# Performance work log

Measured on AMD Instinct MI355X. Metric: run time of the kernel, lower is better.

Reference implementation:

```python
import jax, jax.numpy as jnp
import numpy as np

KH, KW = 5, 5  # kernel; stride=1, padding=0, dilation=1 per init_kwargs


def _unfold(x, kh, kw):
    # torch.nn.functional.unfold with stride=1, pad=0, dil=1, channel-major
    # ordering: out channel index = c*kh*kw + i*kw + j
    B, C, H, W = x.shape
    oh, ow = H - kh + 1, W - kw + 1
    patches = jnp.stack(
        [x[:, :, i:i + oh, j:j + ow] for i in range(kh) for j in range(kw)],
        axis=2,
    )  # [B, C, kh*kw, oh, ow]
    return patches.reshape(B, C * kh * kw, oh, ow)


def _sample_spikes(inp_conv, T):
    # multinomial(replacement=True) over the Cf channel dim per (b, x, y)
    logits = jnp.log(inp_conv.transpose(0, 2, 3, 1))  # [B, OH, OW, Cf]
    B, OH, OW, _ = logits.shape
    return jax.random.categorical(
        jax.random.key(42), logits[:, None], axis=-1, shape=(B, T, OH, OW)
    )  # [B, T, OH, OW] int


def setup_inputs() -> dict:
    key = jax.random.key(0)
    ks = jax.random.split(key, 6)
    B, C, H, W = 32, 24, 28, 28
    OH, OW = 24, 24
    Hn = 128  # number of hidden neurons
    T = 96    # number of spikes
    Cf = C * KH * KW  # 600
    return {
        "input": jax.random.uniform(ks[0], (B, C, H, W), jnp.float32, 0.01, 1.0),
        "epsilon_xy": jax.random.uniform(ks[1], (OH, OW, KH, KW), jnp.float32, 0.1, 1.0),
        "epsilon_0": jax.random.uniform(ks[2], (1,), jnp.float32, 0.5, 1.0),
        "epsilon_t": jax.random.uniform(ks[3], (T,), jnp.float32, 0.5, 1.0),
        "weights": jax.random.uniform(ks[4], (Cf, Hn), jnp.float32, 0.0, 1.0),
        "h_initial": jax.random.uniform(ks[5], (Hn,), jnp.float32, 0.5, 1.0),
        "number_of_spikes": T,
    }


def reference(input, epsilon_xy, epsilon_0, epsilon_t, weights, h_initial,
              number_of_spikes):
    T = int(number_of_spikes)
    B, C = input.shape[0], input.shape[1]
    inp_conv = _unfold(input, KH, KW)              # [B, Cf, OH, OW]
    spikes = _sample_spikes(inp_conv, T)           # [B, T, OH, OW]
    OH, OW = spikes.shape[2], spikes.shape[3]

    # epsilon_xy_convolved: value independent of input channel c,
    # index c*KH*KW + k -> epsilon_xy[x, y] flat at k. Stored as [OH, OW, Cf].
    eps_conv = jnp.tile(epsilon_xy.reshape(OH, OW, KH * KW), (1, 1, C))
    eps0 = epsilon_0[0]

    # Normalized recurrence: g = h / epsilon_scale (exactly equivalent to the
    # original h/epsilon_scale bookkeeping, including the overflow-rescale branch):
    #   g' = (g + eps_sub * (W[s]*g) / sum(W[s]*g)) / (1 + eps_sub)
    Hn = h_initial.shape[0]
    g0 = jnp.broadcast_to(h_initial, (B, OH, OW, Hn)).astype(jnp.float32)

    def step(g, xs):
        s, et = xs                                  # s: [B, OH, OW]
        wg = weights[s] * g                         # [B, OH, OW, Hn]
        denom = jnp.sum(wg, axis=-1, keepdims=True)  # [B, OH, OW, 1]
        eps = jnp.take_along_axis(eps_conv[None], s[..., None], axis=-1)
        eps_sub = eps * (et * eps0)                 # [B, OH, OW, 1]
        factor = jnp.nan_to_num(eps_sub / denom, nan=0.0, posinf=0.0, neginf=0.0)
        g = (g + wg * factor) / (1.0 + eps_sub)
        return g, None

    g, _ = jax.lax.scan(step, g0, (jnp.moveaxis(spikes, 1, 0), epsilon_t[:T]))
    return jnp.moveaxis(g, 3, 1)                    # [B, Hn, OH, OW]
```

## Files before the change

### kernel.cpp

```cpp
#include <hip/hip_runtime.h>
#include <stdint.h>

constexpr int Bn = 32, Cc = 24, Hh = 28, Ww = 28;
constexpr int OHt = 24, OWt = 24;
constexpr int CF = 600, HN = 128, TT = 96;
constexpr int NPIX = OHt * OWt;
constexpr int NSAMP = Bn * TT * NPIX;
constexpr int NLOG = Bn * Cc * Hh * Ww;

__device__ __forceinline__ uint32_t threefry_0_42_pre(uint32_t x1) {
  const uint32_t ks1 = 42u, ks2 = 0x1BD11BF0u;
  uint32_t x0 = x1;
  x1 = __builtin_rotateleft32(x1, 13) ^ x0;
  x0 += x1; x1 = __builtin_rotateleft32(x1, 15) ^ x0;
  x0 += x1; x1 = __builtin_rotateleft32(x1, 26) ^ x0;
  x0 += x1; x1 = __builtin_rotateleft32(x1,  6) ^ x0;
  x0 += ks1; x1 += ks2 + 1u;
  x0 += x1; x1 = __builtin_rotateleft32(x1, 17) ^ x0;
  x0 += x1; x1 = __builtin_rotateleft32(x1, 29) ^ x0;
  x0 += x1; x1 = __builtin_rotateleft32(x1, 16) ^ x0;
  x0 += x1; x1 = __builtin_rotateleft32(x1, 24) ^ x0;
  x0 += ks2; x1 += 2u;
  x0 += x1; x1 = __builtin_rotateleft32(x1, 13) ^ x0;
  x0 += x1; x1 = __builtin_rotateleft32(x1, 15) ^ x0;
  x0 += x1; x1 = __builtin_rotateleft32(x1, 26) ^ x0;
  x0 += x1; x1 = __builtin_rotateleft32(x1,  6) ^ x0;
  x1 += ks1 + 3u;
  x0 += x1; x1 = __builtin_rotateleft32(x1, 17) ^ x0;
  x0 += x1; x1 = __builtin_rotateleft32(x1, 29) ^ x0;
  x0 += x1; x1 = __builtin_rotateleft32(x1, 16) ^ x0;
  x0 += x1; x1 = __builtin_rotateleft32(x1, 24) ^ x0;
  x0 += ks1; x1 += ks2 + 4u;
  x0 += x1; x1 = __builtin_rotateleft32(x1, 13) ^ x0;
  x0 += x1; x1 = __builtin_rotateleft32(x1, 15) ^ x0;
  x0 += x1; x1 = __builtin_rotateleft32(x1, 26) ^ x0;
  x0 += x1; x1 = __builtin_rotateleft32(x1,  6) ^ x0;
  x0 += ks2; x1 += 5u;
  return x0 ^ x1;
}

__global__ __launch_bounds__(256) void k_log(const float* __restrict__ in,
                                             float* __restrict__ lp) {
  int i = blockIdx.x * 256 + threadIdx.x;
  if (i < NLOG) lp[i] = logf(in[i]);
}

__global__ __launch_bounds__(256) void k_lpmax(const float* __restrict__ lp,
                                               float* __restrict__ out) {
  int pid = blockIdx.x * 256 + threadIdx.x;
  if (pid >= Bn * NPIX) return;
  int y = pid % OWt;
  int x = (pid / OWt) % OHt;
  int b = pid / NPIX;
  const float* p = lp + (b * Cc) * (Hh * Ww) + x * Ww + y;
  float m = -3.0e38f;
  for (int c = 0; c < Cc; ++c) {
    const float* pc = p + c * (Hh * Ww);
    #pragma unroll
    for (int ki = 0; ki < 5; ++ki)
      #pragma unroll
      for (int kj = 0; kj < 5; ++kj) m = fmaxf(m, pc[ki * Ww + kj]);
  }
  out[pid] = m;
}

__device__ __forceinline__ uint32_t mkthr(float bgap) {
  float g3 = bgap - 0.00390625f;
  float e1 = __expf(-g3) * 1.0000153f;
  float ul = __expf(-e1) * 0.9999847f;
  int kt = (int)(ul * 8388608.0f) - 64;
  return (kt < 1) ? 0u : ((uint32_t)kt << 9);
}

constexpr int NBIN = 640;

__device__ __forceinline__ void upd(uint32_t bits, float lp, float lpmax,
                                    int cf, float& best, int& bi,
                                    uint32_t& thr, const uint32_t* tab) {
  if (bits < thr) return;
  uint32_t key = bits >> 9;
  float f = __uint_as_float(key | 0x3f800000u) - 1.0f;
  float u = (f == 0.0f) ? 1.17549435e-38f : f;
  float l1 = logf(u);
  float v = -logf(-l1) + lp;
  if (v > best) {
    best = v;
    bi = cf;
    float bg = v - lpmax;
    int bin = (int)__builtin_fmaf(bg, 32.0f, 255.0f);
    if (bin < 0) thr = 0u;
    else thr = tab[bin > (NBIN - 1) ? (NBIN - 1) : bin];
  }
}

__global__ __launch_bounds__(256) void k_sample(const float* __restrict__ logp,
                                                const float* __restrict__ lpmaxa,
                                                int* __restrict__ spikes) {
  __shared__ uint32_t thr_tab[NBIN];
  for (int i = threadIdx.x; i < NBIN; i += 256)
    thr_tab[i] = mkthr(__builtin_fmaf((float)i, 0.03125f, -8.0f));
  __syncthreads();

  int tid = blockIdx.x * 256 + threadIdx.x;
  int y = tid % OWt;
  int x = (tid / OWt) % OHt;
  int t = (tid / NPIX) % 48;
  int b = tid / (NPIX * 48);
  int sid1 = ((b * TT + t) * OHt + x) * OWt + y;
  int sid2 = sid1 + 48 * NPIX;
  uint32_t base1 = (uint32_t)sid1 * 600u + 42u;
  uint32_t base2 = (uint32_t)sid2 * 600u + 42u;
  const float* lpb = logp + (b * Cc) * (Hh * Ww) + x * Ww + y;
  float lpmax = lpmaxa[(b * OHt + x) * OWt + y];
  float best1 = -1e30f, best2 = -1e30f;
  int bi1 = 0, bi2 = 0;
  uint32_t thr1 = 0u, thr2 = 0u;
  int cf = 0;
  #pragma unroll 1
  for (int c = 0; c < Cc; ++c) {
    const float* lpc = lpb + c * (Hh * Ww);
    #pragma unroll
    for (int ki = 0; ki < 5; ++ki) {
      #pragma unroll
      for (int kj = 0; kj < 5; ++kj) {
        float lp = lpc[ki * Ww + kj];
        uint32_t bits1 = threefry_0_42_pre(base1 + (uint32_t)cf);
        uint32_t bits2 = threefry_0_42_pre(base2 + (uint32_t)cf);
        upd(bits1, lp, lpmax, cf, best1, bi1, thr1, thr_tab);
        upd(bits2, lp, lpmax, cf, best2, bi2, thr2, thr_tab);
        ++cf;
      }
    }
  }
  spikes[sid1] = bi1;
  spikes[sid2] = bi2;
}

__global__ __launch_bounds__(256) void k_recur(
    const int* __restrict__ spikes, const float* __restrict__ weights,
    const float* __restrict__ eps_xy, const float* __restrict__ eps_t,
    const float* __restrict__ eps0p, const float* __restrict__ h_init,
    float* __restrict__ out) {
  int wid = blockIdx.x * 4 + (threadIdx.x >> 6);
  int lane = threadIdx.x & 63;
  int y = wid % OWt;
  int x = (wid / OWt) % OHt;
  int b = wid / NPIX;
  float g0 = h_init[lane];
  float g1 = h_init[lane + 64];
  float e0 = eps0p[0];
  const int* sp = spikes + (b * TT) * NPIX + x * OWt + y;
  const float* ex = eps_xy + (x * OWt + y) * 25;
  for (int t = 0; t < TT; ++t) {
    int s = sp[t * NPIX];
    const float* wr = weights + s * HN;
    float wg0 = wr[lane] * g0;
    float wg1 = wr[lane + 64] * g1;
    float sum = wg0 + wg1;
    #pragma unroll
    for (int off = 32; off > 0; off >>= 1) sum += __shfl_xor(sum, off, 64);
    float es = ex[s % 25] * (eps_t[t] * e0);
    float factor = es / sum;
    if (!__builtin_isfinite(factor)) factor = 0.0f;
    float d = 1.0f + es;
    g0 = (g0 + wg0 * factor) / d;
    g1 = (g1 + wg1 * factor) / d;
  }
  out[((b * HN + lane) * OHt + x) * OWt + y] = g0;
  out[((b * HN + lane + 64) * OHt + x) * OWt + y] = g1;
}

extern "C" void kernel_launch(void* const* d_in, const int* in_sizes, int n_in,
                              void* d_out, int out_size, void* d_ws, size_t ws_size,
                              hipStream_t stream) {
  const float* input   = (const float*)d_in[0];
  const float* eps_xy  = (const float*)d_in[1];
  const float* eps0    = (const float*)d_in[2];
  const float* eps_t   = (const float*)d_in[3];
  const float* weights = (const float*)d_in[4];
  const float* h_init  = (const float*)d_in[5];

  float* logp = (float*)d_ws;
  int* spikes = (int*)((char*)d_ws + NLOG * sizeof(float));
  float* lpmax = (float*)d_out;

  k_log<<<(NLOG + 255) / 256, 256, 0, stream>>>(input, logp);
  k_lpmax<<<(Bn * NPIX + 255) / 256, 256, 0, stream>>>(logp, lpmax);
  k_sample<<<(NSAMP / 2) / 256, 256, 0, stream>>>(logp, lpmax, spikes);
  k_recur<<<(Bn * NPIX) / 4, 256, 0, stream>>>(spikes, weights, eps_xy, eps_t,
                                               eps0, h_init, (float*)d_out);
}
```

Before: 2.381 ms.

## Replace exact running argmax with approximate candidate filtering and exact resolve pass

The Gumbel-max sampling loop now keeps a running bound built from fast log2 approximations instead of exact logf values. It uses that bound to pick a threshold per element and records the indices of candidates that pass in a shared-memory list. A second pass recomputes exact values for only those candidates, falling back to a full rescan if the list overflows. This removes the separate lpmax kernel and most exact-log work on the hot path, at the cost of shared-memory stores, per-element table lookups, a partly rolled inner loop, and a redundant threefry recomputation in the resolve pass.

```diff
diff --git a/kernel.cpp b/kernel.cpp
--- a/kernel.cpp
+++ b/kernel.cpp
@@ -7,6 +7,8 @@
 constexpr int NPIX = OHt * OWt;
 constexpr int NSAMP = Bn * TT * NPIX;
 constexpr int NLOG = Bn * Cc * Hh * Ww;
+constexpr int NBIN = 640;
+constexpr int KREC = 24;
 
 __device__ __forceinline__ uint32_t threefry_0_42_pre(uint32_t x1) {
   const uint32_t ks1 = 42u, ks2 = 0x1BD11BF0u;
@@ -45,25 +47,6 @@
   if (i < NLOG) lp[i] = logf(in[i]);
 }
 
-__global__ __launch_bounds__(256) void k_lpmax(const float* __restrict__ lp,
-                                               float* __restrict__ out) {
-  int pid = blockIdx.x * 256 + threadIdx.x;
-  if (pid >= Bn * NPIX) return;
-  int y = pid % OWt;
-  int x = (pid / OWt) % OHt;
-  int b = pid / NPIX;
-  const float* p = lp + (b * Cc) * (Hh * Ww) + x * Ww + y;
-  float m = -3.0e38f;
-  for (int c = 0; c < Cc; ++c) {
-    const float* pc = p + c * (Hh * Ww);
-    #pragma unroll
-    for (int ki = 0; ki < 5; ++ki)
-      #pragma unroll
-      for (int kj = 0; kj < 5; ++kj) m = fmaxf(m, pc[ki * Ww + kj]);
-  }
-  out[pid] = m;
-}
-
 __device__ __forceinline__ uint32_t mkthr(float bgap) {
   float g3 = bgap - 0.00390625f;
   float e1 = __expf(-g3) * 1.0000153f;
@@ -72,31 +55,71 @@
   return (kt < 1) ? 0u : ((uint32_t)kt << 9);
 }
 
-constexpr int NBIN = 640;
-
-__device__ __forceinline__ void upd(uint32_t bits, float lp, float lpmax,
-                                    int cf, float& best, int& bi,
-                                    uint32_t& thr, const uint32_t* tab) {
-  if (bits < thr) return;
+__device__ __forceinline__ float exact_v(uint32_t bits, float lp) {
   uint32_t key = bits >> 9;
   float f = __uint_as_float(key | 0x3f800000u) - 1.0f;
   float u = (f == 0.0f) ? 1.17549435e-38f : f;
   float l1 = logf(u);
-  float v = -logf(-l1) + lp;
-  if (v > best) {
-    best = v;
-    bi = cf;
-    float bg = v - lpmax;
-    int bin = (int)__builtin_fmaf(bg, 32.0f, 255.0f);
-    if (bin < 0) thr = 0u;
-    else thr = tab[bin > (NBIN - 1) ? (NBIN - 1) : bin];
-  }
+  return -logf(-l1) + lp;
+}
+
+__device__ __forceinline__ void rec_upd(uint32_t bits, float lp, float& bA32,
+                                        int& cnt, uint16_t (*recs)[256],
+                                        const uint32_t* __restrict__ tab,
+                                        int cf) {
+  float t = __builtin_fmaf(lp, -32.0f, bA32);
+  t = fminf(fmaxf(t, 0.0f), 639.0f);
+  uint32_t thr = tab[(int)t];
+  if (bits >= thr) {
+    uint32_t key = bits >> 9;
+    float f = __uint_as_float(key | 0x3f800000u) - 1.0f;
+    float u = (f == 0.0f) ? 1.17549435e-38f : f;
+    float lg = __log2f(u);
+    float n = __log2f(-lg);
+    float vh = __builtin_fmaf(-0.6931471805599453f, n, lp);
+    bA32 = fmaxf(bA32, __builtin_fmaf(vh, 32.0f, 266.7284135f));
+    int slot = cnt < KREC - 1 ? cnt : KREC - 1;
+    recs[slot][threadIdx.x] = (uint16_t)cf;
+    ++cnt;
+  }
+}
+
+__device__ __forceinline__ int resolve(int cnt, const uint16_t (*recs)[256],
+                                       uint32_t base,
+                                       const float* __restrict__ lpb) {
+  float best = -1e30f;
+  int bi = 0;
+  if (cnt <= KREC) {
+    for (int j = 0; j < cnt; ++j) {
+      int cf = recs[j][threadIdx.x];
+      int c = cf / 25;
+      int r = cf - c * 25;
+      int ki = r / 5;
+      int kj = r - ki * 5;
+      float lp = lpb[c * (Hh * Ww) + ki * Ww + kj];
+      float v = exact_v(threefry_0_42_pre(base + (uint32_t)cf), lp);
+      if (v > best) { best = v; bi = cf; }
+    }
+  } else {
+    int cf = 0;
+    for (int c = 0; c < Cc; ++c) {
+      const float* lpc = lpb + c * (Hh * Ww);
+      for (int ki = 0; ki < 5; ++ki)
+        for (int kj = 0; kj < 5; ++kj) {
+          float v = exact_v(threefry_0_42_pre(base + (uint32_t)cf),
+                            lpc[ki * Ww + kj]);
+          if (v > best) { best = v; bi = cf; }
+          ++cf;
+        }
+    }
+  }
+  return bi;
 }
 
 __global__ __launch_bounds__(256) void k_sample(const float* __restrict__ logp,
-                                                const float* __restrict__ lpmaxa,
                                                 int* __restrict__ spikes) {
   __shared__ uint32_t thr_tab[NBIN];
+  __shared__ uint16_t rec[2][KREC][256];
   for (int i = threadIdx.x; i < NBIN; i += 256)
     thr_tab[i] = mkthr(__builtin_fmaf((float)i, 0.03125f, -8.0f));
   __syncthreads();
@@ -111,29 +134,27 @@
   uint32_t base1 = (uint32_t)sid1 * 600u + 42u;
   uint32_t base2 = (uint32_t)sid2 * 600u + 42u;
   const float* lpb = logp + (b * Cc) * (Hh * Ww) + x * Ww + y;
-  float lpmax = lpmaxa[(b * OHt + x) * OWt + y];
-  float best1 = -1e30f, best2 = -1e30f;
-  int bi1 = 0, bi2 = 0;
-  uint32_t thr1 = 0u, thr2 = 0u;
+  float bA1 = -3.0e38f, bA2 = -3.0e38f;
+  int cnt1 = 0, cnt2 = 0;
   int cf = 0;
   #pragma unroll 1
   for (int c = 0; c < Cc; ++c) {
     const float* lpc = lpb + c * (Hh * Ww);
-    #pragma unroll
+    #pragma unroll 1
     for (int ki = 0; ki < 5; ++ki) {
       #pragma unroll
       for (int kj = 0; kj < 5; ++kj) {
         float lp = lpc[ki * Ww + kj];
         uint32_t bits1 = threefry_0_42_pre(base1 + (uint32_t)cf);
         uint32_t bits2 = threefry_0_42_pre(base2 + (uint32_t)cf);
-        upd(bits1, lp, lpmax, cf, best1, bi1, thr1, thr_tab);
-        upd(bits2, lp, lpmax, cf, best2, bi2, thr2, thr_tab);
+        rec_upd(bits1, lp, bA1, cnt1, rec[0], thr_tab, cf);
+        rec_upd(bits2, lp, bA2, cnt2, rec[1], thr_tab, cf);
         ++cf;
       }
     }
   }
-  spikes[sid1] = bi1;
-  spikes[sid2] = bi2;
+  spikes[sid1] = resolve(cnt1, rec[0], base1, lpb);
+  spikes[sid2] = resolve(cnt2, rec[1], base2, lpb);
 }
 
 __global__ __launch_bounds__(256) void k_recur(
@@ -182,11 +203,9 @@
 
   float* logp = (float*)d_ws;
   int* spikes = (int*)((char*)d_ws + NLOG * sizeof(float));
-  float* lpmax = (float*)d_out;
 
   k_log<<<(NLOG + 255) / 256, 256, 0, stream>>>(input, logp);
-  k_lpmax<<<(Bn * NPIX + 255) / 256, 256, 0, stream>>>(logp, lpmax);
-  k_sample<<<(NSAMP / 2) / 256, 256, 0, stream>>>(logp, lpmax, spikes);
+  k_sample<<<(NSAMP / 2) / 256, 256, 0, stream>>>(logp, spikes);
   k_recur<<<(Bn * NPIX) / 4, 256, 0, stream>>>(spikes, weights, eps_xy, eps_t,
                                                eps0, h_init, (float*)d_out);
 }
```

Measured after the change: 2.376 ms. Within noise of the previous version (-0.2%).

## Sample four spikes per thread with fast log2 and exact fallback on ties

Applied to the files above, without the earlier changes.

The sampling kernel now evaluates four time steps per thread instead of two, so each logit load is shared across more samples and half as many threads are launched. It replaces the precise logf Gumbel evaluation with fast __log2f approximations and tracks the runner-up value. When the winner's margin over the runner-up is below a small threshold, it recomputes the argmax with a noinline exact logf routine so the result matches the reference. The intent is to cut transcendental cost in the hot loop, at the price of more register pressure, fewer threads in flight and an occasional divergent exact-recompute path.

```diff
diff --git a/kernel.cpp b/kernel.cpp
--- a/kernel.cpp
+++ b/kernel.cpp
@@ -7,6 +7,11 @@
 constexpr int NPIX = OHt * OWt;
 constexpr int NSAMP = Bn * TT * NPIX;
 constexpr int NLOG = Bn * Cc * Hh * Ww;
+constexpr int NBIN = 640;
+
+constexpr float MARGIN = 2.44140625e-4f;
+constexpr float LN2 = 0.6931471805599453f;
+constexpr float CGUM = 0.36651292058166433f;
 
 __device__ __forceinline__ uint32_t threefry_0_42_pre(uint32_t x1) {
   const uint32_t ks1 = 42u, ks2 = 0x1BD11BF0u;
@@ -72,25 +77,33 @@
   return (kt < 1) ? 0u : ((uint32_t)kt << 9);
 }
 
-constexpr int NBIN = 640;
-
-__device__ __forceinline__ void upd(uint32_t bits, float lp, float lpmax,
-                                    int cf, float& best, int& bi,
-                                    uint32_t& thr, const uint32_t* tab) {
-  if (bits < thr) return;
+__device__ __forceinline__ float exact_v(uint32_t bits, float lp) {
   uint32_t key = bits >> 9;
   float f = __uint_as_float(key | 0x3f800000u) - 1.0f;
   float u = (f == 0.0f) ? 1.17549435e-38f : f;
   float l1 = logf(u);
-  float v = -logf(-l1) + lp;
-  if (v > best) {
-    best = v;
-    bi = cf;
-    float bg = v - lpmax;
-    int bin = (int)__builtin_fmaf(bg, 32.0f, 255.0f);
-    if (bin < 0) thr = 0u;
-    else thr = tab[bin > (NBIN - 1) ? (NBIN - 1) : bin];
-  }
+  return -logf(-l1) + lp;
+}
+
+__device__ __attribute__((noinline)) int exact_argmax(
+    uint32_t base, const float* __restrict__ lpb) {
+  float best = -1e30f;
+  int bi = 0;
+  int cf = 0;
+  #pragma unroll 1
+  for (int c = 0; c < Cc; ++c) {
+    const float* lpc = lpb + c * (Hh * Ww);
+    #pragma unroll 1
+    for (int ki = 0; ki < 5; ++ki)
+      #pragma unroll
+      for (int kj = 0; kj < 5; ++kj) {
+        float v = exact_v(threefry_0_42_pre(base + (uint32_t)cf),
+                          lpc[ki * Ww + kj]);
+        if (v > best) { best = v; bi = cf; }
+        ++cf;
+      }
+  }
+  return bi;
 }
 
 __global__ __launch_bounds__(256) void k_sample(const float* __restrict__ logp,
@@ -104,36 +117,68 @@
   int tid = blockIdx.x * 256 + threadIdx.x;
   int y = tid % OWt;
   int x = (tid / OWt) % OHt;
-  int t = (tid / NPIX) % 48;
-  int b = tid / (NPIX * 48);
-  int sid1 = ((b * TT + t) * OHt + x) * OWt + y;
-  int sid2 = sid1 + 48 * NPIX;
-  uint32_t base1 = (uint32_t)sid1 * 600u + 42u;
-  uint32_t base2 = (uint32_t)sid2 * 600u + 42u;
+  int t = (tid / NPIX) % 24;
+  int b = tid / (NPIX * 24);
+  int sid0 = ((b * TT + t) * OHt + x) * OWt + y;
+  uint32_t ctr0 = (uint32_t)sid0 * 600u + 42u;
   const float* lpb = logp + (b * Cc) * (Hh * Ww) + x * Ww + y;
   float lpmax = lpmaxa[(b * OHt + x) * OWt + y];
-  float best1 = -1e30f, best2 = -1e30f;
-  int bi1 = 0, bi2 = 0;
-  uint32_t thr1 = 0u, thr2 = 0u;
+  float K = __builtin_fmaf(-32.0f, lpmax, 255.0f + 32.0f * CGUM);
+
+  float bA0 = -1e30f, bA1 = -1e30f, bA2 = -1e30f, bA3 = -1e30f;
+  float sA0 = -2e30f, sA1 = -2e30f, sA2 = -2e30f, sA3 = -2e30f;
+  int bi0 = 0, bi1 = 0, bi2 = 0, bi3 = 0;
+  uint32_t th0 = 0u, th1 = 0u, th2 = 0u, th3 = 0u;
+
+#define AUPD(kk, BITS, BA, SA, BI, TH)                                      \
+  if ((BITS) >= (TH)) {                                                     \
+    uint32_t key = (BITS) >> 9;                                             \
+    float f = __uint_as_float(key | 0x3f800000u) - 1.0f;                    \
+    float u = (f == 0.0f) ? 1.17549435e-38f : f;                            \
+    float lg = __log2f(u);                                  \
+    float n = __log2f(-lg);                                                 \
+    float vh = __builtin_fmaf(-LN2, n, lp);                 \
+    float nb = fmaxf(BA, vh);                                               \
+    SA = fmaxf(SA, fminf(BA, vh));                                          \
+    if (vh > BA) BI = cf;                                                   \
+    BA = nb;                                                                \
+    float bx = __builtin_fmaf(nb, 32.0f, K);                                \
+    bx = fminf(fmaxf(bx, 0.0f), 639.0f);                                    \
+    TH = thr_tab[(int)bx];                                                  \
+  }
+
   int cf = 0;
   #pragma unroll 1
   for (int c = 0; c < Cc; ++c) {
     const float* lpc = lpb + c * (Hh * Ww);
-    #pragma unroll
+    #pragma unroll 1
     for (int ki = 0; ki < 5; ++ki) {
       #pragma unroll
       for (int kj = 0; kj < 5; ++kj) {
         float lp = lpc[ki * Ww + kj];
-        uint32_t bits1 = threefry_0_42_pre(base1 + (uint32_t)cf);
-        uint32_t bits2 = threefry_0_42_pre(base2 + (uint32_t)cf);
-        upd(bits1, lp, lpmax, cf, best1, bi1, thr1, thr_tab);
-        upd(bits2, lp, lpmax, cf, best2, bi2, thr2, thr_tab);
+        uint32_t c0 = ctr0 + (uint32_t)cf;
+        uint32_t bb0 = threefry_0_42_pre(c0);
+        uint32_t bb1 = threefry_0_42_pre(c0 + 8294400u);
+        uint32_t bb2 = threefry_0_42_pre(c0 + 16588800u);
+        uint32_t bb3 = threefry_0_42_pre(c0 + 24883200u);
+        AUPD(0, bb0, bA0, sA0, bi0, th0)
+        AUPD(1, bb1, bA1, sA1, bi1, th1)
+        AUPD(2, bb2, bA2, sA2, bi2, th2)
+        AUPD(3, bb3, bA3, sA3, bi3, th3)
         ++cf;
       }
     }
   }
-  spikes[sid1] = bi1;
-  spikes[sid2] = bi2;
+#undef AUPD
+
+  int* sp0 = spikes + sid0;
+  sp0[0] = (bA0 - sA0 >= MARGIN) ? bi0 : exact_argmax(ctr0, lpb);
+  sp0[24 * NPIX] =
+      (bA1 - sA1 >= MARGIN) ? bi1 : exact_argmax(ctr0 + 8294400u, lpb);
+  sp0[48 * NPIX] =
+      (bA2 - sA2 >= MARGIN) ? bi2 : exact_argmax(ctr0 + 16588800u, lpb);
+  sp0[72 * NPIX] =
+      (bA3 - sA3 >= MARGIN) ? bi3 : exact_argmax(ctr0 + 24883200u, lpb);
 }
 
 __global__ __launch_bounds__(256) void k_recur(
@@ -186,7 +231,7 @@
 
   k_log<<<(NLOG + 255) / 256, 256, 0, stream>>>(input, logp);
   k_lpmax<<<(Bn * NPIX + 255) / 256, 256, 0, stream>>>(logp, lpmax);
-  k_sample<<<(NSAMP / 2) / 256, 256, 0, stream>>>(logp, lpmax, spikes);
+  k_sample<<<(NSAMP / 4) / 256, 256, 0, stream>>>(logp, lpmax, spikes);
   k_recur<<<(Bn * NPIX) / 4, 256, 0, stream>>>(spikes, weights, eps_xy, eps_t,
                                                eps0, h_init, (float*)d_out);
 }
```

Result: slower. 2.721 ms (+14.3%).
